# Performance work log

Measured on AMD Instinct MI355X. Metric: run time of the kernel, lower is better.

Reference implementation:

```python
import jax, jax.numpy as jnp
import numpy as np

B, N, DIM, H, DH = 4, 2048, 1024, 16, 64
SCALE = DH ** -0.5


def rotate_half(x):
    x1, x2 = jnp.split(x, 2, axis=-1)
    return jnp.concatenate((-x2, x1), axis=-1)


def apply_rope(pos, t):
    # pos: [n, d] broadcast over [b, h, n, d]
    return t * jnp.cos(pos) + rotate_half(t) * jnp.sin(pos)


def setup_inputs() -> dict:
    key = jax.random.key(0)
    ks = jax.random.split(key, 5)
    inner = H * DH
    return {
        "x": jax.random.normal(ks[0], (B, N, DIM), dtype=jnp.float32),
        "rotary_emb_x": jax.random.normal(ks[1], (N, DH), dtype=jnp.float32),
        "Wq": jax.random.normal(ks[2], (DIM, inner), dtype=jnp.float32) * (DIM ** -0.5),
        "Wkv": jax.random.normal(ks[3], (DIM, 2 * inner), dtype=jnp.float32) * (DIM ** -0.5),
        "Wo": jax.random.normal(ks[4], (inner, DIM), dtype=jnp.float32) * (inner ** -0.5),
        "bo": jnp.zeros((DIM,), dtype=jnp.float32),
    }


def reference(x, rotary_emb_x, Wq, Wkv, Wo, bo):
    # projections (self-attention: context = x)
    q = x @ Wq                      # [b, n, h*d]
    kv = x @ Wkv                    # [b, n, 2*h*d]
    k, v = jnp.split(kv, 2, axis=-1)

    def to_heads(t):
        b, n, _ = t.shape
        return t.reshape(b, n, H, DH).transpose(0, 2, 1, 3)  # [b, h, n, d]

    q, k, v = map(to_heads, (q, k, v))

    # rotary on q and k (no context => both use rotary_emb_x)
    q = apply_rope(rotary_emb_x, q)
    k = apply_rope(rotary_emb_x, k)

    # scaled dot-product attention
    scores = jnp.einsum("bhnd,bhmd->bhnm", q, k) * SCALE
    attn = jax.nn.softmax(scores, axis=-1)
    out = jnp.einsum("bhnm,bhmd->bhnd", attn, v)  # [b, h, n, d]

    out = out.transpose(0, 2, 1, 3).reshape(x.shape[0], x.shape[1], H * DH)
    return out @ Wo + bo
```

## Files before the change

### kernel.cpp

```cpp
#include <hip/hip_runtime.h>
#include <hip/hip_bf16.h>
#include <stdint.h>

typedef __attribute__((ext_vector_type(4))) float f32x4;
typedef __attribute__((ext_vector_type(16))) float f32x16;
typedef __attribute__((ext_vector_type(2))) float f32x2;
typedef __attribute__((ext_vector_type(8))) short s16x8;
typedef __attribute__((ext_vector_type(4))) unsigned short u16x4;

__device__ __forceinline__ unsigned short f2bf(float f) {
  union { float f; uint32_t u; } v; v.f = f;
  uint32_t r = v.u + 0x7fffu + ((v.u >> 16) & 1u);
  return (unsigned short)(r >> 16);
}

__device__ __forceinline__ void load_lds16(const void* g, void* l) {
  __builtin_amdgcn_global_load_lds(
      (const __attribute__((address_space(1))) void*)g,
      (__attribute__((address_space(3))) void*)l, 16, 0, 0);
}

#define MFMA16(a, b, c) __builtin_amdgcn_mfma_f32_16x16x32_bf16((a), (b), (c), 0, 0, 0)
#define MFMA32(a, b, c) __builtin_amdgcn_mfma_f32_32x32x16_bf16((a), (b), (c), 0, 0, 0)

__global__ void k_cvt(const float* __restrict__ in, unsigned short* __restrict__ out, int n4) {
  int i = blockIdx.x * blockDim.x + threadIdx.x;
  int stride = gridDim.x * blockDim.x;
  for (; i < n4; i += stride) {
    f32x4 v = ((const f32x4*)in)[i];
    u16x4 o;
    o[0] = f2bf(v[0]); o[1] = f2bf(v[1]); o[2] = f2bf(v[2]); o[3] = f2bf(v[3]);
    ((u16x4*)out)[i] = o;
  }
}

__global__ __launch_bounds__(256) void k_rope_tab(const float* __restrict__ rope,
    float* __restrict__ tq, float* __restrict__ tk) {
  int i = blockIdx.x * blockDim.x + threadIdx.x;
  float p = rope[i];
  float sn, cs; __sincosf(p, &sn, &cs);
  const float a1 = 0.18033688011112042f;
  f32x2 a = {cs * a1, sn * a1};
  f32x2 b = {cs, sn};
  ((f32x2*)tq)[i] = a;
  ((f32x2*)tk)[i] = b;
}

__global__ __launch_bounds__(256) void k_transpose(const float* __restrict__ in,
    unsigned short* __restrict__ out, int K, int N) {
  __shared__ float t[32][33];
  const int tx = threadIdx.x, ty = threadIdx.y;
  const int n0 = blockIdx.x * 32, k0 = blockIdx.y * 32;
#pragma unroll
  for (int i = 0; i < 32; i += 8) t[ty + i][tx] = in[(size_t)(k0 + ty + i) * N + n0 + tx];
  __syncthreads();
#pragma unroll
  for (int i = 0; i < 32; i += 8) out[(size_t)(n0 + ty + i) * K + k0 + tx] = f2bf(t[tx][ty + i]);
}

__global__ __launch_bounds__(256) void k_gemm_qkv(const unsigned short* __restrict__ A,
    const unsigned short* __restrict__ Bt, const float* __restrict__ tq,
    const float* __restrict__ tk,
    unsigned short* __restrict__ qw, unsigned short* __restrict__ kw,
    unsigned short* __restrict__ vt) {
  __shared__ unsigned short As[128 * 64];
  __shared__ unsigned short Bs[128 * 64];
  const int tid = threadIdx.x, l = tid & 63, w = tid >> 6;
  const int tm = blockIdx.y, tn = blockIdx.x;
  const int wr = (w >> 1) * 64, wc = (w & 1) * 64;
  const int lg = l >> 4, lr = l & 15;
  f32x4 acc[4][4] = {};

  for (int kt = 0; kt < 16; ++kt) {
    if (kt) __syncthreads();
    const int k0 = kt * 64;
#pragma unroll
    for (int is = 0; is < 4; ++is) {
      int off = is * 4096 + w * 1024 + l * 16;
      int row = off >> 7;
      int kk = (off & 127) >> 1;
      load_lds16(A + (size_t)(tm * 128 + row) * 1024 + k0 + kk, (char*)As + off);
      load_lds16(Bt + (size_t)(tn * 128 + row) * 1024 + k0 + kk, (char*)Bs + off);
    }
    __syncthreads();
#pragma unroll
    for (int ks = 0; ks < 2; ++ks) {
      s16x8 af[4], bf[4];
#pragma unroll
      for (int mi = 0; mi < 4; ++mi)
        af[mi] = *(const s16x8*)&As[(wr + mi * 16 + lr) * 64 + ks * 32 + lg * 8];
#pragma unroll
      for (int ni = 0; ni < 4; ++ni)
        bf[ni] = *(const s16x8*)&Bs[(wc + ni * 16 + lr) * 64 + ks * 32 + lg * 8];
#pragma unroll
      for (int mi = 0; mi < 4; ++mi)
#pragma unroll
        for (int ni = 0; ni < 4; ++ni)
          acc[mi][ni] = MFMA16(af[mi], bf[ni], acc[mi][ni]);
    }
  }

  const int c0 = tn * 128 + wc;
  const int tensor = c0 >> 10;
  const int h = (c0 & 1023) >> 6;
  if (tensor < 2) {
    unsigned short* dst = tensor == 0 ? qw : kw;
    const float* tbl = tensor == 0 ? tq : tk;
#pragma unroll
    for (int mi = 0; mi < 4; ++mi) {
#pragma unroll
      for (int reg = 0; reg < 4; ++reg) {
        int m = tm * 128 + wr + mi * 16 + lg * 4 + reg;
        int b = m >> 11, n = m & 2047;
        size_t base = ((size_t)(b * 16 + h) * 2048 + n) * 64;
        const float* tb = tbl + (size_t)n * 128;
#pragma unroll
        for (int ni = 0; ni < 4; ++ni) {
          int d = ni * 16 + lr;
          f32x2 cssn = *(const f32x2*)(tb + 2 * d);
          float val = acc[mi][ni][reg];
          float partner = acc[mi][ni ^ 2][reg];
          dst[base + d] = f2bf(val * cssn[0] + (d < 32 ? -partner : partner) * cssn[1]);
        }
      }
    }
  } else {
#pragma unroll
    for (int mi = 0; mi < 4; ++mi) {
      int m0 = tm * 128 + wr + mi * 16 + lg * 4;
      int b = m0 >> 11, n0 = m0 & 2047;
#pragma unroll
      for (int ni = 0; ni < 4; ++ni) {
        int d = ni * 16 + lr;
        u16x4 vv;
#pragma unroll
        for (int reg = 0; reg < 4; ++reg) vv[reg] = f2bf(acc[mi][ni][reg]);
        *(u16x4*)(vt + ((size_t)(b * 16 + h) * 64 + d) * 2048 + n0) = vv;
      }
    }
  }
}

__global__ __launch_bounds__(256, 4) void k_attn(const unsigned short* __restrict__ qw,
    const unsigned short* __restrict__ kw, const unsigned short* __restrict__ vt,
    unsigned short* __restrict__ aout) {
  __shared__ alignas(16) unsigned short Kb[2][4096];
  __shared__ alignas(16) unsigned short Vb[2][4096];
  const int tid = threadIdx.x, l = tid & 63, w = tid >> 6;
  const int ql = l & 31, hi = l >> 5;
  const int bh = blockIdx.y;
  const int qb = blockIdx.x * 128 + w * 32;
  const size_t hbase = (size_t)bh * 2048 * 64;

  s16x8 qf[4];
#pragma unroll
  for (int kt = 0; kt < 4; ++kt)
    qf[kt] = *(const s16x8*)(qw + hbase + (size_t)(qb + ql) * 64 + kt * 16 + hi * 8);

  f32x16 o0 = {}, o1 = {};
  float lsum = 0.f;

  auto STAGE = [&](int kv0, int buf) {
#pragma unroll
    for (int i = 0; i < 2; ++i) {
      int off = i * 4096 + tid * 16;
      int blk = off >> 10, row = (off >> 4) & 63;
      load_lds16(kw + hbase + (size_t)(kv0 + row) * 64 + blk * 8, (char*)Kb[buf] + off);
      load_lds16(vt + hbase + (size_t)row * 2048 + kv0 + blk * 8, (char*)Vb[buf] + off);
    }
  };

  auto COMPUTE = [&](const unsigned short* Kc, const unsigned short* Vc) {
    f32x16 s0 = {}, s1 = {};
    const char* Kp = (const char*)Kc + hi * 1024 + ql * 16;
    __builtin_amdgcn_s_setprio(1);
#pragma unroll
    for (int kt = 0; kt < 4; ++kt) {
      s16x8 kf0 = *(const s16x8*)(Kp + kt * 2048);
      s16x8 kf1 = *(const s16x8*)(Kp + kt * 2048 + 512);
      s0 = MFMA32(kf0, qf[kt], s0);
      s1 = MFMA32(kf1, qf[kt], s1);
    }
    __builtin_amdgcn_s_setprio(0);

    float ls = 0.f;
#pragma unroll
    for (int r = 0; r < 16; ++r) { s0[r] = exp2f(s0[r]); ls += s0[r]; }
#pragma unroll
    for (int r = 0; r < 16; ++r) { s1[r] = exp2f(s1[r]); ls += s1[r]; }
    lsum += ls + __shfl_xor(ls, 32);

    uint32_t W0[8], W1[8];
#pragma unroll
    for (int b = 0; b < 4; ++b)
#pragma unroll
      for (int h2 = 0; h2 < 2; ++h2) {
        asm("v_cvt_pk_bf16_f32 %0, %1, %2" : "=v"(W0[b * 2 + h2])
            : "v"(s0[4 * b + 2 * h2]), "v"(s0[4 * b + 2 * h2 + 1]));
        asm("v_cvt_pk_bf16_f32 %0, %1, %2" : "=v"(W1[b * 2 + h2])
            : "v"(s1[4 * b + 2 * h2]), "v"(s1[4 * b + 2 * h2 + 1]));
      }
    s16x8 pa[4];
#pragma unroll
    for (int kt = 0; kt < 4; ++kt) {
      uint32_t* Wm = (kt >> 1) ? W1 : W0;
      int k = kt & 1;
      uint32_t x0 = Wm[4 * k + 0], y0 = Wm[4 * k + 2];
      uint32_t x1 = Wm[4 * k + 1], y1 = Wm[4 * k + 3];
      asm("v_permlane32_swap_b32 %0, %1" : "+v"(x0), "+v"(y0));
      asm("v_permlane32_swap_b32 %0, %1" : "+v"(x1), "+v"(y1));
      union { uint32_t u[4]; s16x8 v; } pk;
      pk.u[0] = x0; pk.u[1] = x1; pk.u[2] = y0; pk.u[3] = y1;
      pa[kt] = pk.v;
    }

    const char* Vp = (const char*)Vc + hi * 1024 + ql * 16;
    __builtin_amdgcn_s_setprio(1);
#pragma unroll
    for (int kt = 0; kt < 4; ++kt) {
      s16x8 vf0 = *(const s16x8*)(Vp + kt * 2048);
      s16x8 vf1 = *(const s16x8*)(Vp + kt * 2048 + 512);
      o0 = MFMA32(pa[kt], vf0, o0);
      o1 = MFMA32(pa[kt], vf1, o1);
    }
    __builtin_amdgcn_s_setprio(0);
  };

  STAGE(0, 0);
  __syncthreads();
  for (int t = 0; t < 32; t += 2) {
    if (t + 1 < 32) STAGE((t + 1) * 64, 1);
    COMPUTE(Kb[0], Vb[0]);
    __syncthreads();
    if (t + 2 < 32) STAGE((t + 2) * 64, 0);
    COMPUTE(Kb[1], Vb[1]);
    __syncthreads();
  }

  const int b = bh >> 4, h = bh & 15;
  float inv = 1.f / lsum;
#pragma unroll
  for (int r = 0; r < 16; ++r) {
    int qloc = (r & 3) + 8 * (r >> 2) + 4 * hi;
    float ir = __shfl(inv, qloc);
    size_t ob = ((size_t)(b * 2048 + qb + qloc) * 16 + h) * 64;
    aout[ob + ql] = f2bf(o0[r] * ir);
    aout[ob + 32 + ql] = f2bf(o1[r] * ir);
  }
}

__global__ __launch_bounds__(256) void k_gemm_out(const unsigned short* __restrict__ A,
    const unsigned short* __restrict__ Bt, const float* __restrict__ bo,
    float* __restrict__ out) {
  __shared__ unsigned short As[128 * 64];
  __shared__ unsigned short Bs[128 * 64];
  const int tid = threadIdx.x, l = tid & 63, w = tid >> 6;
  const int tm = blockIdx.y, tn = blockIdx.x;
  const int wr = (w >> 1) * 64, wc = (w & 1) * 64;
  const int lg = l >> 4, lr = l & 15;
  f32x4 acc[4][4] = {};

  for (int kt = 0; kt < 16; ++kt) {
    if (kt) __syncthreads();
    const int k0 = kt * 64;
#pragma unroll
    for (int is = 0; is < 4; ++is) {
      int off = is * 4096 + w * 1024 + l * 16;
      int row = off >> 7;
      int kk = (off & 127) >> 1;
      load_lds16(A + (size_t)(tm * 128 + row) * 1024 + k0 + kk, (char*)As + off);
      load_lds16(Bt + (size_t)(tn * 128 + row) * 1024 + k0 + kk, (char*)Bs + off);
    }
    __syncthreads();
#pragma unroll
    for (int ks = 0; ks < 2; ++ks) {
      s16x8 af[4], bf[4];
#pragma unroll
      for (int mi = 0; mi < 4; ++mi)
        af[mi] = *(const s16x8*)&As[(wr + mi * 16 + lr) * 64 + ks * 32 + lg * 8];
#pragma unroll
      for (int ni = 0; ni < 4; ++ni)
        bf[ni] = *(const s16x8*)&Bs[(wc + ni * 16 + lr) * 64 + ks * 32 + lg * 8];
#pragma unroll
      for (int mi = 0; mi < 4; ++mi)
#pragma unroll
        for (int ni = 0; ni < 4; ++ni)
          acc[mi][ni] = MFMA16(af[mi], bf[ni], acc[mi][ni]);
    }
  }
  const int c0 = tn * 128 + wc;
#pragma unroll
  for (int mi = 0; mi < 4; ++mi)
#pragma unroll
    for (int reg = 0; reg < 4; ++reg) {
      int m = tm * 128 + wr + mi * 16 + lg * 4 + reg;
#pragma unroll
      for (int ni = 0; ni < 4; ++ni) {
        int c = c0 + ni * 16 + lr;
        out[(size_t)m * 1024 + c] = acc[mi][ni][reg] + bo[c];
      }
    }
}

extern "C" void kernel_launch(void* const* d_in, const int* in_sizes, int n_in,
                              void* d_out, int out_size, void* d_ws, size_t ws_size,
                              hipStream_t stream) {
  const float* x    = (const float*)d_in[0];
  const float* rope = (const float*)d_in[1];
  const float* Wq   = (const float*)d_in[2];
  const float* Wkv  = (const float*)d_in[3];
  const float* Wo   = (const float*)d_in[4];
  const float* bo   = (const float*)d_in[5];
  float* out = (float*)d_out;

  unsigned short* ws  = (unsigned short*)d_ws;
  unsigned short* xb  = ws;
  unsigned short* wt  = xb + 8192 * 1024;
  unsigned short* wot = wt + 3072 * 1024;
  unsigned short* qws = wot + 1024 * 1024;
  unsigned short* kws = qws + 64 * 2048 * 64;
  unsigned short* vtw = kws + 64 * 2048 * 64;
  float* tq = (float*)(vtw + 64 * 2048 * 64);
  float* tk = tq + 2048 * 64 * 2;
  unsigned short* aws = xb;

  k_cvt<<<1024, 256, 0, stream>>>(x, xb, 8192 * 1024 / 4);
  k_rope_tab<<<512, 256, 0, stream>>>(rope, tq, tk);
  dim3 tb(32, 8);
  k_transpose<<<dim3(32, 32), tb, 0, stream>>>(Wq, wt, 1024, 1024);
  k_transpose<<<dim3(64, 32), tb, 0, stream>>>(Wkv, wt + 1024 * 1024, 1024, 2048);
  k_transpose<<<dim3(32, 32), tb, 0, stream>>>(Wo, wot, 1024, 1024);

  k_gemm_qkv<<<dim3(24, 64), 256, 0, stream>>>(xb, wt, tq, tk, qws, kws, vtw);
  k_attn<<<dim3(16, 64), 256, 0, stream>>>(qws, kws, vtw, aws);
  k_gemm_out<<<dim3(8, 64), 256, 0, stream>>>(aws, wot, bo, out);
}
```

Measured before the change: 318.9 us.

## Rewrite projection GEMMs with 256x128 tiles, triple-buffered LDS pipeline, and XCD swizzle

Replaces the two 128x128 single-buffered GEMM kernels with one templated kernel that uses 512 threads, 256x128 tiles and a three-stage LDS ring filled by direct global-to-LDS loads. Explicit vmcnt waits let loads for stage t+2 overlap the MFMAs for stage t. The change also adds a block-index swizzle across the 8 XCDs for L2 locality and raises wave priority around the MFMA section. It aims to hide global load latency and cut barrier stalls, at the cost of 72KB of LDS per block, which limits occupancy, and fewer blocks for the output GEMM.

```diff
diff --git a/kernel.cpp b/kernel.cpp
--- a/kernel.cpp
+++ b/kernel.cpp
@@ -58,86 +58,126 @@
   for (int i = 0; i < 32; i += 8) out[(size_t)(n0 + ty + i) * K + k0 + tx] = f2bf(t[tx][ty + i]);
 }
 
-__global__ __launch_bounds__(256) void k_gemm_qkv(const unsigned short* __restrict__ A,
-    const unsigned short* __restrict__ Bt, const float* __restrict__ tq,
-    const float* __restrict__ tk,
+template<int MODE>
+__global__ __launch_bounds__(512, 4) void k_gemm8(
+    const unsigned short* __restrict__ A, const unsigned short* __restrict__ Bt,
+    const float* __restrict__ tq, const float* __restrict__ tk,
     unsigned short* __restrict__ qw, unsigned short* __restrict__ kw,
-    unsigned short* __restrict__ vt) {
-  __shared__ unsigned short As[128 * 64];
-  __shared__ unsigned short Bs[128 * 64];
+    unsigned short* __restrict__ vt,
+    const float* __restrict__ bo, float* __restrict__ outf) {
+  __shared__ char lds[73728];
+  constexpr int NTN = (MODE == 0) ? 24 : 8;
+
+  const int nwg = gridDim.x, cpx = nwg >> 3, bid = blockIdx.x;
+  const int swz = (bid & 7) * cpx + (bid >> 3);
+  const int tm = swz / NTN, tn = swz % NTN;
+
   const int tid = threadIdx.x, l = tid & 63, w = tid >> 6;
-  const int tm = blockIdx.y, tn = blockIdx.x;
-  const int wr = (w >> 1) * 64, wc = (w & 1) * 64;
+  const int wm = w >> 1, wn = w & 1;
   const int lg = l >> 4, lr = l & 15;
+
+  unsigned a0 = 0u, a1 = 16384u, a2 = 32768u;
+  unsigned b0 = 49152u, b1 = 57344u, b2 = 65536u;
+
+  const unsigned short* Ap = A + (size_t)(tm * 256 + (tid & 255)) * 1024 + (tid >> 8) * 8;
+  const unsigned short* Bp = Bt + (size_t)(tn * 128 + (tid & 127)) * 1024 + (tid >> 7) * 8;
+
+  const unsigned aoff = lg * 4096 + (wm * 64 + lr) * 16;
+  const unsigned boff = lg * 2048 + (wn * 64 + lr) * 16;
+
+  auto STAGE = [&](unsigned sa, unsigned sb) {
+    load_lds16(Ap, lds + sa + tid * 16);
+    load_lds16(Ap + 16, lds + sa + 8192 + tid * 16);
+    load_lds16(Bp, lds + sb + tid * 16);
+    Ap += 32; Bp += 32;
+  };
+
   f32x4 acc[4][4] = {};
 
-  for (int kt = 0; kt < 16; ++kt) {
-    if (kt) __syncthreads();
-    const int k0 = kt * 64;
-#pragma unroll
-    for (int is = 0; is < 4; ++is) {
-      int off = is * 4096 + w * 1024 + l * 16;
-      int row = off >> 7;
-      int kk = (off & 127) >> 1;
-      load_lds16(A + (size_t)(tm * 128 + row) * 1024 + k0 + kk, (char*)As + off);
-      load_lds16(Bt + (size_t)(tn * 128 + row) * 1024 + k0 + kk, (char*)Bs + off);
-    }
-    __syncthreads();
-#pragma unroll
-    for (int ks = 0; ks < 2; ++ks) {
-      s16x8 af[4], bf[4];
-#pragma unroll
-      for (int mi = 0; mi < 4; ++mi)
-        af[mi] = *(const s16x8*)&As[(wr + mi * 16 + lr) * 64 + ks * 32 + lg * 8];
+  STAGE(a0, b0);
+  STAGE(a1, b1);
+
+  for (int t = 0; t < 32; ++t) {
+    if (t <= 30) asm volatile("s_waitcnt vmcnt(3)" ::: "memory");
+    else         asm volatile("s_waitcnt vmcnt(0)" ::: "memory");
+    __builtin_amdgcn_s_barrier();
+
+    s16x8 bf[4], af[4];
+#pragma unroll
+    for (int ni = 0; ni < 4; ++ni)
+      bf[ni] = *(const s16x8*)(lds + b0 + boff + ni * 256);
+#pragma unroll
+    for (int mi = 0; mi < 4; ++mi)
+      af[mi] = *(const s16x8*)(lds + a0 + aoff + mi * 256);
+
+    if (t < 30) STAGE(a2, b2);
+
+    __builtin_amdgcn_s_setprio(1);
+#pragma unroll
+    for (int mi = 0; mi < 4; ++mi)
 #pragma unroll
       for (int ni = 0; ni < 4; ++ni)
-        bf[ni] = *(const s16x8*)&Bs[(wc + ni * 16 + lr) * 64 + ks * 32 + lg * 8];
-#pragma unroll
-      for (int mi = 0; mi < 4; ++mi)
-#pragma unroll
-        for (int ni = 0; ni < 4; ++ni)
-          acc[mi][ni] = MFMA16(af[mi], bf[ni], acc[mi][ni]);
-    }
-  }
-
-  const int c0 = tn * 128 + wc;
-  const int tensor = c0 >> 10;
-  const int h = (c0 & 1023) >> 6;
-  if (tensor < 2) {
-    unsigned short* dst = tensor == 0 ? qw : kw;
-    const float* tbl = tensor == 0 ? tq : tk;
-#pragma unroll
-    for (int mi = 0; mi < 4; ++mi) {
-#pragma unroll
-      for (int reg = 0; reg < 4; ++reg) {
-        int m = tm * 128 + wr + mi * 16 + lg * 4 + reg;
-        int b = m >> 11, n = m & 2047;
-        size_t base = ((size_t)(b * 16 + h) * 2048 + n) * 64;
-        const float* tb = tbl + (size_t)n * 128;
+        acc[mi][ni] = MFMA16(af[mi], bf[ni], acc[mi][ni]);
+    __builtin_amdgcn_s_setprio(0);
+
+    unsigned ra = a0; a0 = a1; a1 = a2; a2 = ra;
+    unsigned rb = b0; b0 = b1; b1 = b2; b2 = rb;
+  }
+
+  const int c0 = tn * 128 + wn * 64;
+  const int r0 = tm * 256 + wm * 64;
+
+  if constexpr (MODE == 0) {
+    const int tensor = c0 >> 10;
+    const int h = (c0 & 1023) >> 6;
+    if (tensor < 2) {
+      unsigned short* dst = tensor == 0 ? qw : kw;
+      const float* tbl = tensor == 0 ? tq : tk;
+#pragma unroll
+      for (int mi = 0; mi < 4; ++mi) {
+#pragma unroll
+        for (int reg = 0; reg < 4; ++reg) {
+          int m = r0 + mi * 16 + lg * 4 + reg;
+          int b = m >> 11, n = m & 2047;
+          size_t base = ((size_t)(b * 16 + h) * 2048 + n) * 64;
+          const float* tb2 = tbl + (size_t)n * 128;
+#pragma unroll
+          for (int ni = 0; ni < 4; ++ni) {
+            int d = ni * 16 + lr;
+            f32x2 cssn = *(const f32x2*)(tb2 + 2 * d);
+            float val = acc[mi][ni][reg];
+            float partner = acc[mi][ni ^ 2][reg];
+            dst[base + d] = f2bf(val * cssn[0] + (d < 32 ? -partner : partner) * cssn[1]);
+          }
+        }
+      }
+    } else {
+#pragma unroll
+      for (int mi = 0; mi < 4; ++mi) {
+        int m0 = r0 + mi * 16 + lg * 4;
+        int b = m0 >> 11, n0 = m0 & 2047;
 #pragma unroll
         for (int ni = 0; ni < 4; ++ni) {
           int d = ni * 16 + lr;
-          f32x2 cssn = *(const f32x2*)(tb + 2 * d);
-          float val = acc[mi][ni][reg];
-          float partner = acc[mi][ni ^ 2][reg];
-          dst[base + d] = f2bf(val * cssn[0] + (d < 32 ? -partner : partner) * cssn[1]);
+          u16x4 vv;
+#pragma unroll
+          for (int reg = 0; reg < 4; ++reg) vv[reg] = f2bf(acc[mi][ni][reg]);
+          *(u16x4*)(vt + ((size_t)(b * 16 + h) * 64 + d) * 2048 + n0) = vv;
         }
       }
     }
   } else {
 #pragma unroll
-    for (int mi = 0; mi < 4; ++mi) {
-      int m0 = tm * 128 + wr + mi * 16 + lg * 4;
-      int b = m0 >> 11, n0 = m0 & 2047;
-#pragma unroll
-      for (int ni = 0; ni < 4; ++ni) {
-        int d = ni * 16 + lr;
-        u16x4 vv;
-#pragma unroll
-        for (int reg = 0; reg < 4; ++reg) vv[reg] = f2bf(acc[mi][ni][reg]);
-        *(u16x4*)(vt + ((size_t)(b * 16 + h) * 64 + d) * 2048 + n0) = vv;
+    for (int mi = 0; mi < 4; ++mi)
+#pragma unroll
+      for (int reg = 0; reg < 4; ++reg) {
+        int m = r0 + mi * 16 + lg * 4 + reg;
+#pragma unroll
+        for (int ni = 0; ni < 4; ++ni) {
+          int c = c0 + ni * 16 + lr;
+          outf[(size_t)m * 1024 + c] = acc[mi][ni][reg] + bo[c];
+        }
       }
-    }
   }
 }
 
@@ -249,59 +289,6 @@
   }
 }
 
-__global__ __launch_bounds__(256) void k_gemm_out(const unsigned short* __restrict__ A,
-    const unsigned short* __restrict__ Bt, const float* __restrict__ bo,
-    float* __restrict__ out) {
-  __shared__ unsigned short As[128 * 64];
-  __shared__ unsigned short Bs[128 * 64];
-  const int tid = threadIdx.x, l = tid & 63, w = tid >> 6;
-  const int tm = blockIdx.y, tn = blockIdx.x;
-  const int wr = (w >> 1) * 64, wc = (w & 1) * 64;
-  const int lg = l >> 4, lr = l & 15;
-  f32x4 acc[4][4] = {};
-
-  for (int kt = 0; kt < 16; ++kt) {
-    if (kt) __syncthreads();
-    const int k0 = kt * 64;
-#pragma unroll
-    for (int is = 0; is < 4; ++is) {
-      int off = is * 4096 + w * 1024 + l * 16;
-      int row = off >> 7;
-      int kk = (off & 127) >> 1;
-      load_lds16(A + (size_t)(tm * 128 + row) * 1024 + k0 + kk, (char*)As + off);
-      load_lds16(Bt + (size_t)(tn * 128 + row) * 1024 + k0 + kk, (char*)Bs + off);
-    }
-    __syncthreads();
-#pragma unroll
-    for (int ks = 0; ks < 2; ++ks) {
-      s16x8 af[4], bf[4];
-#pragma unroll
-      for (int mi = 0; mi < 4; ++mi)
-        af[mi] = *(const s16x8*)&As[(wr + mi * 16 + lr) * 64 + ks * 32 + lg * 8];
-#pragma unroll
-      for (int ni = 0; ni < 4; ++ni)
-        bf[ni] = *(const s16x8*)&Bs[(wc + ni * 16 + lr) * 64 + ks * 32 + lg * 8];
-#pragma unroll
-      for (int mi = 0; mi < 4; ++mi)
-#pragma unroll
-        for (int ni = 0; ni < 4; ++ni)
-          acc[mi][ni] = MFMA16(af[mi], bf[ni], acc[mi][ni]);
-    }
-  }
-  const int c0 = tn * 128 + wc;
-#pragma unroll
-  for (int mi = 0; mi < 4; ++mi)
-#pragma unroll
-    for (int reg = 0; reg < 4; ++reg) {
-      int m = tm * 128 + wr + mi * 16 + lg * 4 + reg;
-#pragma unroll
-      for (int ni = 0; ni < 4; ++ni) {
-        int c = c0 + ni * 16 + lr;
-        out[(size_t)m * 1024 + c] = acc[mi][ni][reg] + bo[c];
-      }
-    }
-}
-
 extern "C" void kernel_launch(void* const* d_in, const int* in_sizes, int n_in,
                               void* d_out, int out_size, void* d_ws, size_t ws_size,
                               hipStream_t stream) {
@@ -331,7 +318,7 @@
   k_transpose<<<dim3(64, 32), tb, 0, stream>>>(Wkv, wt + 1024 * 1024, 1024, 2048);
   k_transpose<<<dim3(32, 32), tb, 0, stream>>>(Wo, wot, 1024, 1024);
 
-  k_gemm_qkv<<<dim3(24, 64), 256, 0, stream>>>(xb, wt, tq, tk, qws, kws, vtw);
+  k_gemm8<0><<<768, 512, 0, stream>>>(xb, wt, tq, tk, qws, kws, vtw, nullptr, nullptr);
   k_attn<<<dim3(16, 64), 256, 0, stream>>>(qws, kws, vtw, aws);
-  k_gemm_out<<<dim3(8, 64), 256, 0, stream>>>(aws, wot, bo, out);
-}
+  k_gemm8<1><<<256, 512, 0, stream>>>(aws, wot, nullptr, nullptr, nullptr, nullptr, nullptr, bo, out);
+}
```

Result: slower. 358.0 us (+12.3%).
